# Kernel tuning notes

Hardware: AMD Instinct MI355X
Metric: run time of the kernel (lower is better)

## Reference

```python
import jax, jax.numpy as jnp
import numpy as np

B, N, DIM = 4, 2048, 1024
H, DH = 16, 64
INNER = H * DH  # 1024
SCALE = DH ** -0.5


def setup_inputs() -> dict:
    key = jax.random.key(0)
    ks = jax.random.split(key, 6)
    s = 0.02
    return {
        "x": jax.random.normal(ks[0], (B, N, DIM), dtype=jnp.float32),
        "Wq": jax.random.normal(ks[1], (DIM, INNER), dtype=jnp.float32) * s,
        "Wk": jax.random.normal(ks[2], (DIM, INNER), dtype=jnp.float32) * s,
        "Wv": jax.random.normal(ks[3], (DIM, INNER), dtype=jnp.float32) * s,
        "Wo": jax.random.normal(ks[4], (INNER, DIM), dtype=jnp.float32) * s,
        "bo": jax.random.normal(ks[5], (DIM,), dtype=jnp.float32) * s,
    }


def reference(x, Wq, Wk, Wv, Wo, bo):
    # q/k/v projections: [B,N,INNER] -> [B,H,N,DH]
    def split_heads(t):
        return t.reshape(B, N, H, DH).transpose(0, 2, 1, 3)

    q = split_heads(x @ Wq)
    k = split_heads(x @ Wk)
    v = split_heads(x @ Wv)

    # scores [B,H,N,N], scaled dot product, softmax over keys (last dim)
    dots = jnp.einsum('bhid,bhjd->bhij', q, k) * SCALE
    attn = jax.nn.softmax(dots, axis=-1)

    out = jnp.einsum('bhij,bhjd->bhid', attn, v)
    out = out.transpose(0, 2, 1, 3).reshape(B, N, INNER)
    return out @ Wo + bo
```

## Files before the change

kernel.cpp:

```cpp
#include <hip/hip_runtime.h>

#define B_SZ   4
#define N_SEQ  2048
#define DIM    1024
#define H_N    16
#define DH     64
#define INNER  1024
#define M_TOK  8192
#define QSCALE 0.1803368801111244f

typedef __attribute__((ext_vector_type(8))) short bf16x8;
typedef __attribute__((ext_vector_type(4))) float f32x4;
typedef __attribute__((ext_vector_type(4))) unsigned int u32x4;

__device__ __forceinline__ unsigned short f2b(float f) {
  union { float f; unsigned u; } v; v.f = f;
  unsigned r = v.u + 0x7fffu + ((v.u >> 16) & 1u);
  return (unsigned short)(r >> 16);
}

__device__ __forceinline__ unsigned cvtpk_bf16(float a, float b) {
  unsigned r;
  asm("v_cvt_pk_bf16_f32 %0, %1, %2" : "=v"(r) : "v"(a), "v"(b));
  return r;
}

__device__ __forceinline__ void gl_lds16(const unsigned short* g, unsigned short* l) {
  __builtin_amdgcn_global_load_lds((const __attribute__((address_space(1))) void*)g,
                                   (__attribute__((address_space(3))) void*)l, 16, 0, 0);
}

__global__ __launch_bounds__(256) void cast_x(const float* __restrict__ x,
                                              unsigned short* __restrict__ xb) {
  int i = (blockIdx.x * 256 + threadIdx.x) * 4;
  float4 v = *(const float4*)(x + i);
  ushort4 o;
  o.x = f2b(v.x); o.y = f2b(v.y); o.z = f2b(v.z); o.w = f2b(v.w);
  *(ushort4*)(xb + i) = o;
}

__global__ __launch_bounds__(256) void trans_w(const float* __restrict__ Wq,
    const float* __restrict__ Wk, const float* __restrict__ Wv,
    const float* __restrict__ Wo, unsigned short* __restrict__ WT) {
  const int z = blockIdx.z;
  const float* W = (z == 0) ? Wq : (z == 1) ? Wk : (z == 2) ? Wv : Wo;
  unsigned short* T = WT + (size_t)z * DIM * INNER;
  __shared__ float tile[64][65];
  const int n0 = blockIdx.x * 64, k0 = blockIdx.y * 64;
  const int tid = threadIdx.x;
#pragma unroll
  for (int it = 0; it < 16; it++) {
    int lin = it * 256 + tid;
    int r = lin >> 6, c = lin & 63;
    tile[r][c] = W[(size_t)(k0 + r) * 1024 + n0 + c];
  }
  __syncthreads();
#pragma unroll
  for (int it = 0; it < 16; it++) {
    int lin = it * 256 + tid;
    int r = lin >> 6, c = lin & 63;
    T[(size_t)(n0 + r) * 1024 + k0 + c] = f2b(tile[c][r]);
  }
}

__global__ __launch_bounds__(256) void qkv_gemm(const unsigned short* __restrict__ xb,
    const unsigned short* __restrict__ WT, unsigned short* __restrict__ QKV) {
  __shared__ __align__(16) unsigned short As[2 * 128 * 32];
  __shared__ __align__(16) unsigned short Bs[2 * 128 * 32];
  const int tid = threadIdx.x;
  const int lane = tid & 63, wv = tid >> 6;
  const int quad = lane >> 4, l16 = lane & 15;
  const int wm = wv >> 1, wn = wv & 1;
  const int m0 = blockIdx.x * 128, n0 = blockIdx.y * 128;
  const unsigned short* Ag = xb + (size_t)m0 * DIM;
  const unsigned short* Bg = WT + (size_t)blockIdx.z * DIM * INNER + (size_t)n0 * DIM;
  unsigned short* Out = QKV + (size_t)blockIdx.z * M_TOK * INNER;

  f32x4 zero = {0.f, 0.f, 0.f, 0.f};
  f32x4 acc[4][4];
#pragma unroll
  for (int i = 0; i < 4; i++)
#pragma unroll
    for (int j = 0; j < 4; j++) acc[i][j] = zero;

  const int lr = lane >> 2, lc = (lane & 3) * 8;
  const int c0 = wv * 2, c1 = wv * 2 + 1;

  for (int k0 = 0; k0 < DIM; k0 += 64) {
    __syncthreads();
#pragma unroll
    for (int h = 0; h < 2; h++) {
      gl_lds16(&Ag[(size_t)(c0 * 16 + lr) * DIM + k0 + h * 32 + lc], &As[h * 4096 + c0 * 512]);
      gl_lds16(&Ag[(size_t)(c1 * 16 + lr) * DIM + k0 + h * 32 + lc], &As[h * 4096 + c1 * 512]);
      gl_lds16(&Bg[(size_t)(c0 * 16 + lr) * DIM + k0 + h * 32 + lc], &Bs[h * 4096 + c0 * 512]);
      gl_lds16(&Bg[(size_t)(c1 * 16 + lr) * DIM + k0 + h * 32 + lc], &Bs[h * 4096 + c1 * 512]);
    }
    __syncthreads();
#pragma unroll
    for (int h = 0; h < 2; h++) {
      bf16x8 af[4], bfr[4];
#pragma unroll
      for (int i = 0; i < 4; i++)
        af[i] = *(const bf16x8*)&As[h * 4096 + (wm * 64 + i * 16 + l16) * 32 + quad * 8];
#pragma unroll
      for (int j = 0; j < 4; j++)
        bfr[j] = *(const bf16x8*)&Bs[h * 4096 + (wn * 64 + j * 16 + l16) * 32 + quad * 8];
#pragma unroll
      for (int i = 0; i < 4; i++)
#pragma unroll
        for (int j = 0; j < 4; j++)
          acc[i][j] = __builtin_amdgcn_mfma_f32_16x16x32_bf16(af[i], bfr[j], acc[i][j], 0, 0, 0);
    }
  }
  if (blockIdx.z != 2) {
    const float cs = (blockIdx.z == 0) ? QSCALE : 1.0f;
#pragma unroll
    for (int i = 0; i < 4; i++) {
#pragma unroll
      for (int j = 0; j < 4; j++) {
        int n = n0 + wn * 64 + j * 16 + l16;
#pragma unroll
        for (int r = 0; r < 4; r++) {
          int m = m0 + wm * 64 + i * 16 + quad * 4 + r;
          Out[(size_t)m * INNER + n] = f2b(acc[i][j][r] * cs);
        }
      }
    }
  } else {
#pragma unroll
    for (int i = 0; i < 4; i++) {
#pragma unroll
      for (int j = 0; j < 4; j++) {
        int n = n0 + wn * 64 + j * 16 + l16;
        int h = n >> 6, dh = n & 63;
        int mbase = m0 + wm * 64 + i * 16 + quad * 4;
        int b = mbase >> 11, nq = mbase & 2047;
        unsigned lo = (unsigned)f2b(acc[i][j][0]) | ((unsigned)f2b(acc[i][j][1]) << 16);
        unsigned hi = (unsigned)f2b(acc[i][j][2]) | ((unsigned)f2b(acc[i][j][3]) << 16);
        uint2 pw; pw.x = lo; pw.y = hi;
        *(uint2*)&Out[((size_t)(b * H_N + h) * DH + dh) * N_SEQ + nq] = pw;
      }
    }
  }
}

#define KT 64
#define LSTR 72

__global__ __launch_bounds__(256, 4) void attn(const unsigned short* __restrict__ Q,
    const unsigned short* __restrict__ K, const unsigned short* __restrict__ VT,
    unsigned short* __restrict__ O) {
  __shared__ __align__(16) unsigned short Ks[KT * LSTR];
  __shared__ __align__(16) unsigned short VTs[DH * LSTR];
  const int tid = threadIdx.x;
  const int lane = tid & 63, w = tid >> 6;
  const int quad = lane >> 4, l16 = lane & 15;
  const int bh = blockIdx.y;
  const int b = bh >> 4, h = bh & 15;
  const int q0 = blockIdx.x * 128;
  const unsigned short* Qp = Q + ((size_t)b * N_SEQ) * INNER + h * DH;
  const unsigned short* Kp = K + ((size_t)b * N_SEQ) * INNER + h * DH;
  const unsigned short* VTp = VT + (size_t)bh * DH * N_SEQ;

  bf16x8 aq[2][2];
#pragma unroll
  for (int qi = 0; qi < 2; qi++) {
    const unsigned short* qr = Qp + (size_t)(q0 + w * 32 + qi * 16 + l16) * INNER;
    aq[qi][0] = *(const bf16x8*)&qr[quad * 8];
    aq[qi][1] = *(const bf16x8*)&qr[32 + quad * 8];
  }

  bf16x8 vone;
#pragma unroll
  for (int j = 0; j < 8; j++) vone[j] = (short)0x3F80;

  f32x4 zero = {0.f, 0.f, 0.f, 0.f};
  f32x4 oacc[2][4];
  f32x4 lacc[2];
#pragma unroll
  for (int qi = 0; qi < 2; qi++) {
    lacc[qi] = zero;
#pragma unroll
    for (int t = 0; t < 4; t++) oacc[qi][t] = zero;
  }

  const int srow = tid >> 3, scol = (tid & 7) * 8;

  for (int k0 = 0; k0 < N_SEQ; k0 += KT) {
    __syncthreads();
#pragma unroll
    for (int p = 0; p < 2; p++)
      *(uint4*)&Ks[(p * 32 + srow) * LSTR + scol] =
          *(const uint4*)&Kp[(size_t)(k0 + p * 32 + srow) * INNER + scol];
#pragma unroll
    for (int p = 0; p < 2; p++)
      *(uint4*)&VTs[(p * 32 + srow) * LSTR + scol] =
          *(const uint4*)&VTp[(size_t)(p * 32 + srow) * N_SEQ + k0 + scol];
    __syncthreads();

#pragma unroll
    for (int half = 0; half < 2; half++) {
      f32x4 s[2][2];
#pragma unroll
      for (int t = 0; t < 2; t++)
#pragma unroll
        for (int qi = 0; qi < 2; qi++) s[t][qi] = zero;

#pragma unroll
      for (int kk = 0; kk < 2; kk++) {
#pragma unroll
        for (int t = 0; t < 2; t++) {
          bf16x8 ka = *(const bf16x8*)&Ks[((half * 2 + t) * 16 + l16) * LSTR + kk * 32 + quad * 8];
#pragma unroll
          for (int qi = 0; qi < 2; qi++)
            s[t][qi] = __builtin_amdgcn_mfma_f32_16x16x32_bf16(ka, aq[qi][kk], s[t][qi], 0, 0, 0);
        }
      }

      bf16x8 pa[2];
#pragma unroll
      for (int qi = 0; qi < 2; qi++) {
#pragma unroll
        for (int t = 0; t < 2; t++)
#pragma unroll
          for (int r = 0; r < 4; r++)
            s[t][qi][r] = __builtin_amdgcn_exp2f(s[t][qi][r]);
        unsigned lo0 = cvtpk_bf16(s[0][qi][0], s[0][qi][1]);
        unsigned hi0 = cvtpk_bf16(s[0][qi][2], s[0][qi][3]);
        unsigned lo1 = cvtpk_bf16(s[1][qi][0], s[1][qi][1]);
        unsigned hi1 = cvtpk_bf16(s[1][qi][2], s[1][qi][3]);
        asm("v_permlane32_swap_b32 %0, %1" : "+v"(lo0), "+v"(lo1));
        asm("v_permlane16_swap_b32 %0, %1" : "+v"(lo0), "+v"(lo1));
        asm("v_permlane32_swap_b32 %0, %1" : "+v"(hi0), "+v"(hi1));
        asm("v_permlane16_swap_b32 %0, %1" : "+v"(hi0), "+v"(hi1));
        u32x4 pk;
        pk.x = lo0; pk.y = hi0; pk.z = lo1; pk.w = hi1;
        pa[qi] = __builtin_bit_cast(bf16x8, pk);
      }

      lacc[0] = __builtin_amdgcn_mfma_f32_16x16x32_bf16(pa[0], vone, lacc[0], 0, 0, 0);
      lacc[1] = __builtin_amdgcn_mfma_f32_16x16x32_bf16(pa[1], vone, lacc[1], 0, 0, 0);
#pragma unroll
      for (int t2 = 0; t2 < 4; t2++) {
        bf16x8 vf = *(const bf16x8*)&VTs[(t2 * 16 + l16) * LSTR + half * 32 + quad * 8];
        oacc[0][t2] = __builtin_amdgcn_mfma_f32_16x16x32_bf16(pa[0], vf, oacc[0][t2], 0, 0, 0);
        oacc[1][t2] = __builtin_amdgcn_mfma_f32_16x16x32_bf16(pa[1], vf, oacc[1][t2], 0, 0, 0);
      }
    }
  }

#pragma unroll
  for (int qi = 0; qi < 2; qi++) {
#pragma unroll
    for (int r = 0; r < 4; r++) {
      float rl = __builtin_amdgcn_rcpf(lacc[qi][r]);
      int qrow = q0 + w * 32 + qi * 16 + quad * 4 + r;
#pragma unroll
      for (int t2 = 0; t2 < 4; t2++) {
        int col = h * DH + t2 * 16 + l16;
        O[((size_t)b * N_SEQ + qrow) * INNER + col] = f2b(oacc[qi][t2][r] * rl);
      }
    }
  }
}

__global__ __launch_bounds__(256) void out_gemm(const unsigned short* __restrict__ Ob,
    const unsigned short* __restrict__ WoT, const float* __restrict__ bo,
    float* __restrict__ out) {
  __shared__ __align__(16) unsigned short As[2 * 128 * 32];
  __shared__ __align__(16) unsigned short Bs[2 * 64 * 32];
  const int tid = threadIdx.x;
  const int lane = tid & 63, wv = tid >> 6;
  const int quad = lane >> 4, l16 = lane & 15;
  const int wm = wv >> 1, wn = wv & 1;
  const int m0 = blockIdx.x * 128, n0 = blockIdx.y * 64;
  const unsigned short* Ag = Ob + (size_t)m0 * INNER;
  const unsigned short* Bg = WoT + (size_t)n0 * INNER;

  f32x4 zero = {0.f, 0.f, 0.f, 0.f};
  f32x4 acc[4][2];
#pragma unroll
  for (int i = 0; i < 4; i++)
#pragma unroll
    for (int j = 0; j < 2; j++) acc[i][j] = zero;

  const int lr = lane >> 2, lc = (lane & 3) * 8;
  const int c0 = wv * 2, c1 = wv * 2 + 1;
  const int cb = wv;

  for (int k0 = 0; k0 < INNER; k0 += 64) {
    __syncthreads();
#pragma unroll
    for (int h = 0; h < 2; h++) {
      gl_lds16(&Ag[(size_t)(c0 * 16 + lr) * INNER + k0 + h * 32 + lc], &As[h * 4096 + c0 * 512]);
      gl_lds16(&Ag[(size_t)(c1 * 16 + lr) * INNER + k0 + h * 32 + lc], &As[h * 4096 + c1 * 512]);
      gl_lds16(&Bg[(size_t)(cb * 16 + lr) * INNER + k0 + h * 32 + lc], &Bs[h * 2048 + cb * 512]);
    }
    __syncthreads();
#pragma unroll
    for (int h = 0; h < 2; h++) {
      bf16x8 af[4], bfr[2];
#pragma unroll
      for (int i = 0; i < 4; i++)
        af[i] = *(const bf16x8*)&As[h * 4096 + (wm * 64 + i * 16 + l16) * 32 + quad * 8];
#pragma unroll
      for (int j = 0; j < 2; j++)
        bfr[j] = *(const bf16x8*)&Bs[h * 2048 + (wn * 32 + j * 16 + l16) * 32 + quad * 8];
#pragma unroll
      for (int i = 0; i < 4; i++)
#pragma unroll
        for (int j = 0; j < 2; j++)
          acc[i][j] = __builtin_amdgcn_mfma_f32_16x16x32_bf16(af[i], bfr[j], acc[i][j], 0, 0, 0);
    }
  }
#pragma unroll
  for (int i = 0; i < 4; i++) {
#pragma unroll
    for (int j = 0; j < 2; j++) {
      int n = n0 + wn * 32 + j * 16 + l16;
      float bias = bo[n];
#pragma unroll
      for (int r = 0; r < 4; r++) {
        int m = m0 + wm * 64 + i * 16 + quad * 4 + r;
        out[(size_t)m * DIM + n] = acc[i][j][r] + bias;
      }
    }
  }
}

extern "C" void kernel_launch(void* const* d_in, const int* in_sizes, int n_in,
                              void* d_out, int out_size, void* d_ws, size_t ws_size,
                              hipStream_t stream) {
  const float* x  = (const float*)d_in[0];
  const float* Wq = (const float*)d_in[1];
  const float* Wk = (const float*)d_in[2];
  const float* Wv = (const float*)d_in[3];
  const float* Wo = (const float*)d_in[4];
  const float* bo = (const float*)d_in[5];

  char* ws = (char*)d_ws;
  unsigned short* xb   = (unsigned short*)ws;
  unsigned short* WT   = (unsigned short*)(ws + (size_t)16777216);
  unsigned short* QKV  = (unsigned short*)(ws + (size_t)25165824);
  unsigned short* Obuf = (unsigned short*)(ws + (size_t)75497472);

  cast_x<<<dim3(8192), 256, 0, stream>>>(x, xb);
  trans_w<<<dim3(16, 16, 4), 256, 0, stream>>>(Wq, Wk, Wv, Wo, WT);
  qkv_gemm<<<dim3(64, 8, 3), 256, 0, stream>>>(xb, WT, QKV);
  attn<<<dim3(16, 64), 256, 0, stream>>>(QKV,
                                         QKV + (size_t)M_TOK * INNER,
                                         QKV + (size_t)2 * M_TOK * INNER,
                                         Obuf);
  out_gemm<<<dim3(64, 16), 256, 0, stream>>>(Obuf, WT + (size_t)3 * DIM * INNER, bo,
                                             (float*)d_out);
}
```

Baseline: 269.9 us.

## Double attention block to 512 threads sharing K/V tiles; batch bf16 pack/permlane asm

The attention kernel now runs 8 waves per block over 256 query rows instead of 4 waves over 128. Each K/V tile staged in LDS is therefore reused by twice as many queries, with one load per thread per tile. This halves the global K/V traffic and the per-block staging overhead. The bf16 conversion and permlane swaps are also merged into a single volatile asm block with explicit s_nop hazards, which may constrain scheduling. Half as many blocks (512) are launched, which reduces the number of resident blocks available on the device.

```diff
diff --git a/kernel.cpp b/kernel.cpp
--- a/kernel.cpp
+++ b/kernel.cpp
@@ -17,12 +17,6 @@
   union { float f; unsigned u; } v; v.f = f;
   unsigned r = v.u + 0x7fffu + ((v.u >> 16) & 1u);
   return (unsigned short)(r >> 16);
-}
-
-__device__ __forceinline__ unsigned cvtpk_bf16(float a, float b) {
-  unsigned r;
-  asm("v_cvt_pk_bf16_f32 %0, %1, %2" : "=v"(r) : "v"(a), "v"(b));
-  return r;
 }
 
 __device__ __forceinline__ void gl_lds16(const unsigned short* g, unsigned short* l) {
@@ -147,7 +141,7 @@
 #define KT 64
 #define LSTR 72
 
-__global__ __launch_bounds__(256, 4) void attn(const unsigned short* __restrict__ Q,
+__global__ __launch_bounds__(512, 4) void attn(const unsigned short* __restrict__ Q,
     const unsigned short* __restrict__ K, const unsigned short* __restrict__ VT,
     unsigned short* __restrict__ O) {
   __shared__ __align__(16) unsigned short Ks[KT * LSTR];
@@ -157,7 +151,7 @@
   const int quad = lane >> 4, l16 = lane & 15;
   const int bh = blockIdx.y;
   const int b = bh >> 4, h = bh & 15;
-  const int q0 = blockIdx.x * 128;
+  const int q0 = blockIdx.x * 256;
   const unsigned short* Qp = Q + ((size_t)b * N_SEQ) * INNER + h * DH;
   const unsigned short* Kp = K + ((size_t)b * N_SEQ) * INNER + h * DH;
   const unsigned short* VTp = VT + (size_t)bh * DH * N_SEQ;
@@ -188,14 +182,10 @@
 
   for (int k0 = 0; k0 < N_SEQ; k0 += KT) {
     __syncthreads();
-#pragma unroll
-    for (int p = 0; p < 2; p++)
-      *(uint4*)&Ks[(p * 32 + srow) * LSTR + scol] =
-          *(const uint4*)&Kp[(size_t)(k0 + p * 32 + srow) * INNER + scol];
-#pragma unroll
-    for (int p = 0; p < 2; p++)
-      *(uint4*)&VTs[(p * 32 + srow) * LSTR + scol] =
-          *(const uint4*)&VTp[(size_t)(p * 32 + srow) * N_SEQ + k0 + scol];
+    *(uint4*)&Ks[srow * LSTR + scol] =
+        *(const uint4*)&Kp[(size_t)(k0 + srow) * INNER + scol];
+    *(uint4*)&VTs[srow * LSTR + scol] =
+        *(const uint4*)&VTp[(size_t)srow * N_SEQ + k0 + scol];
     __syncthreads();
 
 #pragma unroll
@@ -225,14 +215,22 @@
 #pragma unroll
           for (int r = 0; r < 4; r++)
             s[t][qi][r] = __builtin_amdgcn_exp2f(s[t][qi][r]);
-        unsigned lo0 = cvtpk_bf16(s[0][qi][0], s[0][qi][1]);
-        unsigned hi0 = cvtpk_bf16(s[0][qi][2], s[0][qi][3]);
-        unsigned lo1 = cvtpk_bf16(s[1][qi][0], s[1][qi][1]);
-        unsigned hi1 = cvtpk_bf16(s[1][qi][2], s[1][qi][3]);
-        asm("v_permlane32_swap_b32 %0, %1" : "+v"(lo0), "+v"(lo1));
-        asm("v_permlane16_swap_b32 %0, %1" : "+v"(lo0), "+v"(lo1));
-        asm("v_permlane32_swap_b32 %0, %1" : "+v"(hi0), "+v"(hi1));
-        asm("v_permlane16_swap_b32 %0, %1" : "+v"(hi0), "+v"(hi1));
+        unsigned lo0, hi0, lo1, hi1;
+        asm volatile(
+            "v_cvt_pk_bf16_f32 %0, %4, %5\n\t"
+            "v_cvt_pk_bf16_f32 %1, %6, %7\n\t"
+            "v_cvt_pk_bf16_f32 %2, %8, %9\n\t"
+            "v_cvt_pk_bf16_f32 %3, %10, %11\n\t"
+            "s_nop 1\n\t"
+            "v_permlane32_swap_b32 %0, %2\n\t"
+            "v_permlane32_swap_b32 %1, %3\n\t"
+            "s_nop 1\n\t"
+            "v_permlane16_swap_b32 %0, %2\n\t"
+            "v_permlane16_swap_b32 %1, %3\n\t"
+            "s_nop 1"
+            : "=&v"(lo0), "=&v"(hi0), "=&v"(lo1), "=&v"(hi1)
+            : "v"(s[0][qi][0]), "v"(s[0][qi][1]), "v"(s[0][qi][2]), "v"(s[0][qi][3]),
+              "v"(s[1][qi][0]), "v"(s[1][qi][1]), "v"(s[1][qi][2]), "v"(s[1][qi][3]));
         u32x4 pk;
         pk.x = lo0; pk.y = hi0; pk.z = lo1; pk.w = hi1;
         pa[qi] = __builtin_bit_cast(bf16x8, pk);
@@ -347,10 +345,10 @@
   cast_x<<<dim3(8192), 256, 0, stream>>>(x, xb);
   trans_w<<<dim3(16, 16, 4), 256, 0, stream>>>(Wq, Wk, Wv, Wo, WT);
   qkv_gemm<<<dim3(64, 8, 3), 256, 0, stream>>>(xb, WT, QKV);
-  attn<<<dim3(16, 64), 256, 0, stream>>>(QKV,
-                                         QKV + (size_t)M_TOK * INNER,
-                                         QKV + (size_t)2 * M_TOK * INNER,
-                                         Obuf);
+  attn<<<dim3(8, 64), 512, 0, stream>>>(QKV,
+                                        QKV + (size_t)M_TOK * INNER,
+                                        QKV + (size_t)2 * M_TOK * INNER,
+                                        Obuf);
   out_gemm<<<dim3(64, 16), 256, 0, stream>>>(Obuf, WT + (size_t)3 * DIM * INNER, bo,
                                              (float*)d_out);
 }
```

After: 269.0 us. Within noise of the previous version (-0.3%).
